# Performance work log

Measured on AMD Instinct MI355X. Metric: run time of the kernel, lower is better.

Reference implementation:

```python
import jax, jax.numpy as jnp
import numpy as np

NUM_CLASSES = 19
EPSILON = 1e-05


def setup_inputs() -> dict:
    key = jax.random.key(0)
    k1, k2 = jax.random.split(key)
    shape = (16, 1024, 1024)
    y_pred = jax.random.randint(k1, shape, 0, NUM_CLASSES, dtype=jnp.int64 if jax.config.read('jax_enable_x64') else jnp.int32)
    y = jax.random.randint(k2, shape, 0, NUM_CLASSES, dtype=y_pred.dtype)
    return {"y_pred": y_pred, "y": y}


def reference(y_pred, y):
    # Flatten label maps; compute all per-class counts in one pass via bincount
    yp = y_pred.reshape(-1)
    yt = y.reshape(-1)
    # count of (y == i)
    count_y = jnp.bincount(yt, length=NUM_CLASSES).astype(jnp.float32)
    # count of (y_pred == i)
    count_p = jnp.bincount(yp, length=NUM_CLASSES).astype(jnp.float32)
    # intersection_i = count(y == i AND y_pred == i): histogram of y where labels agree
    agree = (yp == yt).astype(jnp.float32)
    inter = jnp.bincount(yt, weights=agree, length=NUM_CLASSES)
    # union_i = |A| + |B| - |A & B|
    union = count_y + count_p - inter
    dice_coeffs = (2.0 * inter + EPSILON) / (union + EPSILON)
    dice_loss = 1.0 - jnp.mean(dice_coeffs)
    return dice_loss
```

## Files before the change

kernel.cpp:

```cpp
#include <hip/hip_runtime.h>

#define NC 19
#define NB (NC * NC)
#define EPS 1e-5f

__global__ __launch_bounds__(256) void joint_hist_kernel(
    const int4* __restrict__ yp, const int4* __restrict__ yt,
    unsigned int* __restrict__ gJ, int n4)
{
    __shared__ unsigned int sJ[4 * NB];
    const int tid = threadIdx.x;
    unsigned int* mine = &sJ[(tid >> 6) * NB];

    for (int i = tid; i < 4 * NB; i += 256) sJ[i] = 0u;
    __syncthreads();

    const int stride = gridDim.x * 256;
    for (int i = blockIdx.x * 256 + tid; i < n4; i += stride) {
        int4 p = yp[i];
        int4 t = yt[i];
        atomicAdd(&mine[t.x * NC + p.x], 1u);
        atomicAdd(&mine[t.y * NC + p.y], 1u);
        atomicAdd(&mine[t.z * NC + p.z], 1u);
        atomicAdd(&mine[t.w * NC + p.w], 1u);
    }
    __syncthreads();

    for (int i = tid; i < NB; i += 256) {
        unsigned int v = sJ[i] + sJ[NB + i] + sJ[2 * NB + i] + sJ[3 * NB + i];
        if (v) atomicAdd(&gJ[i], v);
    }
}

__global__ __launch_bounds__(64) void dice_final_kernel(
    const unsigned int* __restrict__ gJ, float* __restrict__ out)
{
    const int lane = threadIdx.x;
    float dice = 0.0f;
    if (lane < NC) {
        float inter = (float)gJ[lane * NC + lane];
        float cy = 0.0f, cp = 0.0f;
        #pragma unroll
        for (int j = 0; j < NC; ++j) {
            cy += (float)gJ[lane * NC + j];
            cp += (float)gJ[j * NC + lane];
        }
        float uni = cy + cp - inter;
        dice = (2.0f * inter + EPS) / (uni + EPS);
    }
    #pragma unroll
    for (int off = 32; off > 0; off >>= 1)
        dice += __shfl_down(dice, off, 64);
    if (lane == 0) out[0] = 1.0f - dice / (float)NC;
}

extern "C" void kernel_launch(void* const* d_in, const int* in_sizes, int n_in,
                              void* d_out, int out_size, void* d_ws, size_t ws_size,
                              hipStream_t stream)
{
    const int4* yp = (const int4*)d_in[0];
    const int4* yt = (const int4*)d_in[1];
    unsigned int* gJ = (unsigned int*)d_ws;
    float* out = (float*)d_out;

    const int n = in_sizes[0];
    const int n4 = n >> 2;

    hipMemsetAsync(d_ws, 0, NB * sizeof(unsigned int), stream);

    const int grid = 1024;
    joint_hist_kernel<<<grid, 256, 0, stream>>>(yp, yt, gJ, n4);
    dice_final_kernel<<<1, 64, 0, stream>>>(gJ, out);
}
```

Measured before the change: 154.6 us.

## Replace LDS atomic joint histogram with register per-class counters and fused finalize

Drops the 19x19 joint histogram built with shared-memory atomics. Each thread now keeps register counters of union contributions (count of y plus count of y_pred) and of intersections for each class, using compare-and-add over all classes. Counters are packed two per 32-bit word, reduced with wave shuffles and LDS, then added atomically to global memory. A last-block ticket computes the dice loss in the same kernel, removing the second launch. This trades LDS atomic contention for about 57 VALU compare-adds per element, and relies on the 16-bit packed partial counts not overflowing.

```diff
diff --git a/kernel.cpp b/kernel.cpp
--- a/kernel.cpp
+++ b/kernel.cpp
@@ -1,57 +1,101 @@
 #include <hip/hip_runtime.h>
 
 #define NC 19
-#define NB (NC * NC)
+#define NPK 20
 #define EPS 1e-5f
 
-__global__ __launch_bounds__(256) void joint_hist_kernel(
+__device__ __forceinline__ void count_one(int t, int p,
+                                          unsigned* __restrict__ u,
+                                          unsigned* __restrict__ itc)
+{
+    int q = (t == p) ? t : NC;
+    #pragma unroll
+    for (int c = 0; c < NC; ++c) {
+        u[c]   += (unsigned)(t == c);
+        u[c]   += (unsigned)(p == c);
+        itc[c] += (unsigned)(q == c);
+    }
+}
+
+__global__ __launch_bounds__(256) void dice_main(
     const int4* __restrict__ yp, const int4* __restrict__ yt,
-    unsigned int* __restrict__ gJ, int n4)
+    unsigned* __restrict__ gU, unsigned* __restrict__ gI,
+    unsigned* __restrict__ ticket, float* __restrict__ out, int n4)
 {
-    __shared__ unsigned int sJ[4 * NB];
-    const int tid = threadIdx.x;
-    unsigned int* mine = &sJ[(tid >> 6) * NB];
-
-    for (int i = tid; i < 4 * NB; i += 256) sJ[i] = 0u;
-    __syncthreads();
+    unsigned u[NC], itc[NC];
+    #pragma unroll
+    for (int c = 0; c < NC; ++c) { u[c] = 0u; itc[c] = 0u; }
 
     const int stride = gridDim.x * 256;
-    for (int i = blockIdx.x * 256 + tid; i < n4; i += stride) {
-        int4 p = yp[i];
-        int4 t = yt[i];
-        atomicAdd(&mine[t.x * NC + p.x], 1u);
-        atomicAdd(&mine[t.y * NC + p.y], 1u);
-        atomicAdd(&mine[t.z * NC + p.z], 1u);
-        atomicAdd(&mine[t.w * NC + p.w], 1u);
+    for (int i = blockIdx.x * 256 + threadIdx.x; i < n4; i += stride) {
+        int4 p4 = yp[i];
+        int4 t4 = yt[i];
+        count_one(t4.x, p4.x, u, itc);
+        count_one(t4.y, p4.y, u, itc);
+        count_one(t4.z, p4.z, u, itc);
+        count_one(t4.w, p4.w, u, itc);
+    }
+
+    unsigned P[NPK];
+    #pragma unroll
+    for (int j = 0; j < 10; ++j) {
+        unsigned bu = (2*j + 1 < NC) ? u[2*j + 1]   : 0u;
+        unsigned bi = (2*j + 1 < NC) ? itc[2*j + 1] : 0u;
+        P[j]      = u[2*j]   | (bu << 16);
+        P[10 + j] = itc[2*j] | (bi << 16);
+    }
+
+    #pragma unroll
+    for (int j = 0; j < NPK; ++j) {
+        #pragma unroll
+        for (int off = 1; off < 64; off <<= 1)
+            P[j] += __shfl_xor(P[j], off, 64);
+    }
+
+    __shared__ unsigned ldsP[4 * NPK];
+    __shared__ unsigned s_old;
+    const int lane = threadIdx.x & 63;
+    const int wv   = threadIdx.x >> 6;
+    if (lane == 0) {
+        #pragma unroll
+        for (int j = 0; j < NPK; ++j) ldsP[wv * NPK + j] = P[j];
     }
     __syncthreads();
 
-    for (int i = tid; i < NB; i += 256) {
-        unsigned int v = sJ[i] + sJ[NB + i] + sJ[2 * NB + i] + sJ[3 * NB + i];
-        if (v) atomicAdd(&gJ[i], v);
+    if (threadIdx.x < NPK) {
+        unsigned lo = 0, hi = 0;
+        #pragma unroll
+        for (int w = 0; w < 4; ++w) {
+            unsigned v = ldsP[w * NPK + threadIdx.x];
+            lo += v & 0xffffu;
+            hi += v >> 16;
+        }
+        const int j = threadIdx.x;
+        unsigned* base = (j < 10) ? gU : gI;
+        const int c0 = (j < 10) ? 2*j : 2*(j - 10);
+        atomicAdd(&base[c0], lo);
+        if (c0 + 1 < NC) atomicAdd(&base[c0 + 1], hi);
     }
-}
 
-__global__ __launch_bounds__(64) void dice_final_kernel(
-    const unsigned int* __restrict__ gJ, float* __restrict__ out)
-{
-    const int lane = threadIdx.x;
-    float dice = 0.0f;
-    if (lane < NC) {
-        float inter = (float)gJ[lane * NC + lane];
-        float cy = 0.0f, cp = 0.0f;
+    __threadfence();
+    __syncthreads();
+    if (threadIdx.x == 0)
+        s_old = __hip_atomic_fetch_add(ticket, 1u, __ATOMIC_ACQ_REL, __HIP_MEMORY_SCOPE_AGENT);
+    __syncthreads();
+    if (s_old == gridDim.x - 1 && threadIdx.x < 64) {
+        float dice = 0.0f;
+        if (lane < NC) {
+            unsigned Uv = __hip_atomic_load(&gU[lane], __ATOMIC_RELAXED, __HIP_MEMORY_SCOPE_AGENT);
+            unsigned Iv = __hip_atomic_load(&gI[lane], __ATOMIC_RELAXED, __HIP_MEMORY_SCOPE_AGENT);
+            float I = (float)Iv;
+            float U = (float)Uv;
+            dice = (2.0f * I + EPS) / ((U - I) + EPS);
+        }
         #pragma unroll
-        for (int j = 0; j < NC; ++j) {
-            cy += (float)gJ[lane * NC + j];
-            cp += (float)gJ[j * NC + lane];
-        }
-        float uni = cy + cp - inter;
-        dice = (2.0f * inter + EPS) / (uni + EPS);
+        for (int off = 32; off > 0; off >>= 1)
+            dice += __shfl_down(dice, off, 64);
+        if (lane == 0) out[0] = 1.0f - dice * (1.0f / (float)NC);
     }
-    #pragma unroll
-    for (int off = 32; off > 0; off >>= 1)
-        dice += __shfl_down(dice, off, 64);
-    if (lane == 0) out[0] = 1.0f - dice / (float)NC;
 }
 
 extern "C" void kernel_launch(void* const* d_in, const int* in_sizes, int n_in,
@@ -60,15 +104,15 @@
 {
     const int4* yp = (const int4*)d_in[0];
     const int4* yt = (const int4*)d_in[1];
-    unsigned int* gJ = (unsigned int*)d_ws;
+    unsigned* gU     = (unsigned*)d_ws;
+    unsigned* gI     = gU + NC;
+    unsigned* ticket = gI + NC;
     float* out = (float*)d_out;
 
-    const int n = in_sizes[0];
+    const int n  = in_sizes[0];
     const int n4 = n >> 2;
 
-    hipMemsetAsync(d_ws, 0, NB * sizeof(unsigned int), stream);
+    hipMemsetAsync(d_ws, 0, (2 * NC + 1) * sizeof(unsigned), stream);
 
-    const int grid = 1024;
-    joint_hist_kernel<<<grid, 256, 0, stream>>>(yp, yt, gJ, n4);
-    dice_final_kernel<<<1, 64, 0, stream>>>(gJ, out);
+    dice_main<<<1024, 256, 0, stream>>>(yp, yt, gU, gI, ticket, out, n4);
 }
```

Result: slower. 321.6 us (+107.9%).

## Fuse final dice reduction via last-block ticket, more LDS copies, 2x unroll

Applied to the files above, without the earlier changes.

Merges the finalize kernel into the histogram kernel: the last block to finish, found with an atomic ticket counter, computes the dice loss. This removes one kernel launch. It also doubles the per-block shared histogram copies to 8 (one per 32 threads) to reduce LDS atomic contention, unrolls the grid-stride loop by two so more loads are in flight, and doubles the grid to 2048 blocks. The costs are more global atomics from more blocks and an extra memset element for the ticket.

```diff
diff --git a/kernel.cpp b/kernel.cpp
--- a/kernel.cpp
+++ b/kernel.cpp
@@ -2,56 +2,80 @@
 
 #define NC 19
 #define NB (NC * NC)
+#define NCOPY 8
 #define EPS 1e-5f
 
-__global__ __launch_bounds__(256) void joint_hist_kernel(
+__global__ __launch_bounds__(256, 8) void dice_main(
     const int4* __restrict__ yp, const int4* __restrict__ yt,
-    unsigned int* __restrict__ gJ, int n4)
+    unsigned* __restrict__ gJ, unsigned* __restrict__ ticket,
+    float* __restrict__ out, int n4)
 {
-    __shared__ unsigned int sJ[4 * NB];
+    __shared__ unsigned sJ[NCOPY * NB];
+    __shared__ unsigned s_old;
     const int tid = threadIdx.x;
-    unsigned int* mine = &sJ[(tid >> 6) * NB];
+    unsigned* mine = &sJ[(tid >> 5) * NB];
 
-    for (int i = tid; i < 4 * NB; i += 256) sJ[i] = 0u;
+    for (int i = tid; i < NCOPY * NB; i += 256) sJ[i] = 0u;
     __syncthreads();
 
     const int stride = gridDim.x * 256;
-    for (int i = blockIdx.x * 256 + tid; i < n4; i += stride) {
-        int4 p = yp[i];
-        int4 t = yt[i];
-        atomicAdd(&mine[t.x * NC + p.x], 1u);
-        atomicAdd(&mine[t.y * NC + p.y], 1u);
-        atomicAdd(&mine[t.z * NC + p.z], 1u);
-        atomicAdd(&mine[t.w * NC + p.w], 1u);
+    int i = blockIdx.x * 256 + tid;
+
+    while (i + stride < n4) {
+        int4 t0 = yt[i];          int4 p0 = yp[i];
+        int4 t1 = yt[i + stride]; int4 p1 = yp[i + stride];
+        atomicAdd(&mine[t0.x * NC + p0.x], 1u);
+        atomicAdd(&mine[t0.y * NC + p0.y], 1u);
+        atomicAdd(&mine[t0.z * NC + p0.z], 1u);
+        atomicAdd(&mine[t0.w * NC + p0.w], 1u);
+        atomicAdd(&mine[t1.x * NC + p1.x], 1u);
+        atomicAdd(&mine[t1.y * NC + p1.y], 1u);
+        atomicAdd(&mine[t1.z * NC + p1.z], 1u);
+        atomicAdd(&mine[t1.w * NC + p1.w], 1u);
+        i += 2 * stride;
+    }
+    if (i < n4) {
+        int4 t0 = yt[i]; int4 p0 = yp[i];
+        atomicAdd(&mine[t0.x * NC + p0.x], 1u);
+        atomicAdd(&mine[t0.y * NC + p0.y], 1u);
+        atomicAdd(&mine[t0.z * NC + p0.z], 1u);
+        atomicAdd(&mine[t0.w * NC + p0.w], 1u);
     }
     __syncthreads();
 
-    for (int i = tid; i < NB; i += 256) {
-        unsigned int v = sJ[i] + sJ[NB + i] + sJ[2 * NB + i] + sJ[3 * NB + i];
-        if (v) atomicAdd(&gJ[i], v);
+    for (int b = tid; b < NB; b += 256) {
+        unsigned v = 0;
+        #pragma unroll
+        for (int c = 0; c < NCOPY; ++c) v += sJ[c * NB + b];
+        if (v) atomicAdd(&gJ[b], v);
     }
-}
 
-__global__ __launch_bounds__(64) void dice_final_kernel(
-    const unsigned int* __restrict__ gJ, float* __restrict__ out)
-{
-    const int lane = threadIdx.x;
-    float dice = 0.0f;
-    if (lane < NC) {
-        float inter = (float)gJ[lane * NC + lane];
-        float cy = 0.0f, cp = 0.0f;
+    __threadfence();
+    __syncthreads();
+    if (tid == 0)
+        s_old = __hip_atomic_fetch_add(ticket, 1u, __ATOMIC_ACQ_REL, __HIP_MEMORY_SCOPE_AGENT);
+    __syncthreads();
+    if (s_old == gridDim.x - 1 && tid < 64) {
+        const int lane = tid;
+        float dice = 0.0f;
+        if (lane < NC) {
+            float inter = 0.0f, cy = 0.0f, cp = 0.0f;
+            #pragma unroll
+            for (int j = 0; j < NC; ++j) {
+                unsigned r = __hip_atomic_load(&gJ[lane * NC + j], __ATOMIC_RELAXED, __HIP_MEMORY_SCOPE_AGENT);
+                unsigned c = __hip_atomic_load(&gJ[j * NC + lane], __ATOMIC_RELAXED, __HIP_MEMORY_SCOPE_AGENT);
+                cy += (float)r;
+                cp += (float)c;
+                if (j == lane) inter = (float)r;
+            }
+            float uni = cy + cp - inter;
+            dice = (2.0f * inter + EPS) / (uni + EPS);
+        }
         #pragma unroll
-        for (int j = 0; j < NC; ++j) {
-            cy += (float)gJ[lane * NC + j];
-            cp += (float)gJ[j * NC + lane];
-        }
-        float uni = cy + cp - inter;
-        dice = (2.0f * inter + EPS) / (uni + EPS);
+        for (int off = 32; off > 0; off >>= 1)
+            dice += __shfl_down(dice, off, 64);
+        if (lane == 0) out[0] = 1.0f - dice * (1.0f / (float)NC);
     }
-    #pragma unroll
-    for (int off = 32; off > 0; off >>= 1)
-        dice += __shfl_down(dice, off, 64);
-    if (lane == 0) out[0] = 1.0f - dice / (float)NC;
 }
 
 extern "C" void kernel_launch(void* const* d_in, const int* in_sizes, int n_in,
@@ -60,15 +84,14 @@
 {
     const int4* yp = (const int4*)d_in[0];
     const int4* yt = (const int4*)d_in[1];
-    unsigned int* gJ = (unsigned int*)d_ws;
+    unsigned* gJ     = (unsigned*)d_ws;
+    unsigned* ticket = gJ + NB;
     float* out = (float*)d_out;
 
-    const int n = in_sizes[0];
+    const int n  = in_sizes[0];
     const int n4 = n >> 2;
 
-    hipMemsetAsync(d_ws, 0, NB * sizeof(unsigned int), stream);
+    hipMemsetAsync(d_ws, 0, (NB + 1) * sizeof(unsigned), stream);
 
-    const int grid = 1024;
-    joint_hist_kernel<<<grid, 256, 0, stream>>>(yp, yt, gJ, n4);
-    dice_final_kernel<<<1, 64, 0, stream>>>(gJ, out);
+    dice_main<<<2048, 256, 0, stream>>>(yp, yt, gJ, ticket, out, n4);
 }
```

Result: slower. 433.1 us (+180.1%).
